# Kernel optimization log

Hardware: AMD Instinct MI355X
Metric: run time of the kernel (lower is better)

## Reference

```python
import jax, jax.numpy as jnp
import numpy as np

N_RAYS = 32768
N_SAMPLES = 1048576
HID = 64
STEP = 0.0005


def _mlp(x, W1, b1, W2, b2, W3, b3):
    h = jax.nn.relu(x @ W1 + b1)
    h = jax.nn.relu(h @ W2 + b2)
    return h @ W3 + b3


def setup_inputs() -> dict:
    key = jax.random.key(0)
    ks = jax.random.split(key, 12)
    rays_o = jax.random.normal(ks[0], (N_RAYS, 3), jnp.float32)
    rays_d = jax.random.normal(ks[1], (N_RAYS, 3), jnp.float32)
    rays_d = rays_d / jnp.linalg.norm(rays_d, axis=-1, keepdims=True)
    t_starts = jax.random.uniform(ks[2], (N_SAMPLES,), jnp.float32, 0.0, 1.5)
    t_ends = t_starts + STEP
    ray_indices = jnp.sort(jax.random.randint(ks[3], (N_SAMPLES,), 0, N_RAYS, jnp.int32))
    def lin(k, fin, fout):
        return jax.random.normal(k, (fin, fout), jnp.float32) / np.sqrt(fin)
    return {
        'rays_o': rays_o, 'rays_d': rays_d,
        't_starts': t_starts, 't_ends': t_ends,
        'ray_indices': ray_indices,
        'W_d1': lin(ks[4], 3, HID), 'b_d1': jnp.zeros((HID,), jnp.float32),
        'W_d2': lin(ks[5], HID, HID), 'b_d2': jnp.zeros((HID,), jnp.float32),
        'W_d3': lin(ks[6], HID, 1), 'b_d3': jnp.zeros((1,), jnp.float32),
        'W_r1': lin(ks[7], 3, HID), 'b_r1': jnp.zeros((HID,), jnp.float32),
        'W_r2': lin(ks[8], HID, HID), 'b_r2': jnp.zeros((HID,), jnp.float32),
        'W_r3': lin(ks[9], HID, 3), 'b_r3': jnp.zeros((3,), jnp.float32),
    }


def reference(rays_o, rays_d, t_starts, t_ends, ray_indices,
              W_d1, b_d1, W_d2, b_d2, W_d3, b_d3,
              W_r1, b_r1, W_r2, b_r2, W_r3, b_r3):
    n_rays = rays_o.shape[0]
    mid = (t_starts + t_ends) * 0.5                      # [S]
    # gather ray origins/dirs per sample, compute positions
    positions = rays_o[ray_indices] + rays_d[ray_indices] * mid[:, None]  # [S,3]
    # density query (NGP decoder stand-in), softplus activation like trunc_exp family
    sigmas = jax.nn.softplus(_mlp(positions, W_d1, b_d1, W_d2, b_d2, W_d3, b_d3))[:, 0]  # [S]
    # render_weight_from_density: segment-wise exclusive cumsum of sigma*dt
    sigma_dt = sigmas * (t_ends - t_starts)              # [S]
    excl_global = jnp.cumsum(sigma_dt) - sigma_dt        # global exclusive cumsum
    per_ray = jax.ops.segment_sum(sigma_dt, ray_indices, num_segments=n_rays)  # [R]
    ray_excl = jnp.cumsum(per_ray) - per_ray             # exclusive cumsum over rays
    within_excl = excl_global - ray_excl[ray_indices]    # exclusive within each ray
    trans = jnp.exp(-within_excl)                        # transmittance
    alphas = 1.0 - jnp.exp(-sigma_dt)
    weights = trans * alphas
    # accumulate_along_rays (scatter-sum over ray_indices)
    opacities = jax.ops.segment_sum(weights, ray_indices, num_segments=n_rays)[:, None]  # [R,1]
    distances = jax.ops.segment_sum(weights * mid, ray_indices, num_segments=n_rays)[:, None]
    # rgb query
    rgbs = jax.nn.sigmoid(_mlp(positions, W_r1, b_r1, W_r2, b_r2, W_r3, b_r3))  # [S,3]
    w_sg = jax.lax.stop_gradient(weights)
    colors = jax.ops.segment_sum(w_sg[:, None] * rgbs, ray_indices, num_segments=n_rays)  # [R,3]
    # eval-mode background composition (nerf.training == False branch)
    rest = jax.lax.stop_gradient(1.0 - opacities)
    distances = distances + 5.0 * rest
    colors = colors + 0.5 * rest
    return colors, distances, opacities
```

## Files before the change

kernel.cpp:

```cpp
#include <hip/hip_runtime.h>
#include <hip/hip_bf16.h>
#include <math.h>

#define N_RAYS   32768
#define N_SAMP   1048576
#define HID      64
#define ITERS    4
#define BLK_A    1024

typedef short bf8 __attribute__((ext_vector_type(8)));
typedef float f4  __attribute__((ext_vector_type(4)));

union BF8U { bf8 v; unsigned u[4]; };

static __device__ __forceinline__ unsigned bfbits(float x) {
    union { __bf16 h; unsigned short s; } c; c.h = (__bf16)x; return (unsigned)c.s;
}
static __device__ __forceinline__ unsigned pk2(float a, float b) {
#if __has_builtin(__builtin_amdgcn_cvt_pk_bf16_f32)
    return __builtin_bit_cast(unsigned, __builtin_amdgcn_cvt_pk_bf16_f32(a, b));
#else
    return bfbits(a) | (bfbits(b) << 16);
#endif
}
static __device__ __forceinline__ unsigned pk2r(float a, float b) {
    return pk2(fmaxf(a, 0.f), fmaxf(b, 0.f));
}
static __device__ __forceinline__ f4 mfma16(bf8 a, bf8 b, f4 c) {
    return __builtin_amdgcn_mfma_f32_16x16x32_bf16(a, b, c, 0, 0, 0);
}

__global__ __launch_bounds__(256, 2) void pass_a(
    const float* __restrict__ rays_o, const float* __restrict__ rays_d,
    const float* __restrict__ t_starts, const float* __restrict__ t_ends,
    const int*   __restrict__ ray_idx,
    const float* __restrict__ Wd1, const float* __restrict__ bd1,
    const float* __restrict__ Wd2, const float* __restrict__ bd2,
    const float* __restrict__ Wd3, const float* __restrict__ bd3,
    const float* __restrict__ Wr1, const float* __restrict__ br1,
    const float* __restrict__ Wr2, const float* __restrict__ br2,
    const float* __restrict__ Wr3, const float* __restrict__ br3,
    float4* __restrict__ ws4, int* __restrict__ start)
{
    const int lane = threadIdx.x & 63;
    const int wv   = (blockIdx.x * blockDim.x + threadIdx.x) >> 6;
    const int q    = lane >> 4;
    const int n    = lane & 15;
    const int qn   = n >> 2, rn = n & 3;
    const int rt   = n & 3;

    bf8 a1d[4], a1r[4];
    #pragma unroll
    for (int t = 0; t < 4; ++t) {
        const int row = 8*qn + 4*(t&1) + rn + 32*(t>>1);
        BF8U fd, fr;
        fd.u[0] = pk2(Wd1[row],       Wd1[HID+row]);
        fd.u[1] = pk2(Wd1[2*HID+row], bd1[row]);
        fd.u[2] = 0u; fd.u[3] = 0u;
        fr.u[0] = pk2(Wr1[row],       Wr1[HID+row]);
        fr.u[1] = pk2(Wr1[2*HID+row], br1[row]);
        fr.u[2] = 0u; fr.u[3] = 0u;
        a1d[t] = fd.v; a1r[t] = fr.v;
    }

    bf8 a2d[4][2], a2r[4][2];
    #pragma unroll
    for (int t = 0; t < 4; ++t) {
        const int row = 8*qn + 4*(t&1) + rn + 32*(t>>1);
        #pragma unroll
        for (int s = 0; s < 2; ++s) {
            BF8U fd, fr;
            #pragma unroll
            for (int dw = 0; dw < 4; ++dw) {
                const int k = 8*q + 2*dw + 32*s;
                fd.u[dw] = pk2(Wd2[k*HID+row], Wd2[(k+1)*HID+row]);
                fr.u[dw] = pk2(Wr2[k*HID+row], Wr2[(k+1)*HID+row]);
            }
            a2d[t][s] = fd.v; a2r[t][s] = fr.v;
        }
    }

    bf8 a3[4];
    #pragma unroll
    for (int s = 0; s < 4; ++s) {
        BF8U f;
        #pragma unroll
        for (int dw = 0; dw < 4; ++dw) {
            const int kg = 32*s + 8*q + 2*dw;
            float va = 0.f, vb = 0.f;
            if (rt == 0 && s < 2) { va = Wd3[kg]; vb = Wd3[kg+1]; }
            else if (rt >= 1 && s >= 2) {
                va = Wr3[(kg-64)*3 + (rt-1)];
                vb = Wr3[(kg-63)*3 + (rt-1)];
            }
            f.u[dw] = pk2(va, vb);
        }
        a3[s] = f.v;
    }

    f4 bias2d[4], bias2r[4];
    #pragma unroll
    for (int t = 0; t < 4; ++t) {
        #pragma unroll
        for (int rr = 0; rr < 4; ++rr) {
            const int row = 8*q + 4*(t&1) + rr + 32*(t>>1);
            bias2d[t][rr] = bd2[row];
            bias2r[t][rr] = br2[row];
        }
    }
    f4 bias3;
    #pragma unroll
    for (int rr = 0; rr < 4; ++rr)
        bias3[rr] = (rr == 0) ? bd3[0] : br3[rr-1];

    const int base0 = wv * (ITERS * 64);

    #pragma unroll 1
    for (int it = 0; it < ITERS; ++it) {
        const int base = base0 + it * 64;
        const int smp  = base + lane;

        const float ts = t_starts[smp], te = t_ends[smp];
        const int   ri = ray_idx[smp];
        const float mid = 0.5f*(ts+te), dt = te - ts;
        const float px = rays_o[3*ri+0] + rays_d[3*ri+0]*mid;
        const float py = rays_o[3*ri+1] + rays_d[3*ri+1]*mid;
        const float pz = rays_o[3*ri+2] + rays_d[3*ri+2]*mid;
        const unsigned p01 = pk2(px, py);
        const unsigned p23 = pk2(pz, 1.0f);

        int rp = __shfl_up(ri, 1, 64);
        if (lane == 0) rp = (smp == 0) ? -1 : ray_idx[smp-1];
        for (int rr = rp + 1; rr <= ri; ++rr) start[rr] = smp;
        if (smp == N_SAMP - 1)
            for (int rr = ri + 1; rr <= N_RAYS; ++rr) start[rr] = N_SAMP;

        f4 mine = {0.f, 0.f, 0.f, 0.f};

        #pragma unroll
        for (int u = 0; u < 4; ++u) {
            BF8U xb;
            xb.u[0] = (q == u) ? p01 : 0u;
            xb.u[1] = (q == u) ? p23 : 0u;
            xb.u[2] = 0u; xb.u[3] = 0u;

            const f4 zero = {0.f, 0.f, 0.f, 0.f};
            f4 d1d[4], d1r[4];
            #pragma unroll
            for (int t = 0; t < 4; ++t) {
                d1d[t] = mfma16(a1d[t], xb.v, zero);
                d1r[t] = mfma16(a1r[t], xb.v, zero);
            }

            bf8 b2d[2], b2r[2];
            #pragma unroll
            for (int s = 0; s < 2; ++s) {
                BF8U pd, pr;
                pd.u[0] = pk2r(d1d[2*s][0],   d1d[2*s][1]);
                pd.u[1] = pk2r(d1d[2*s][2],   d1d[2*s][3]);
                pd.u[2] = pk2r(d1d[2*s+1][0], d1d[2*s+1][1]);
                pd.u[3] = pk2r(d1d[2*s+1][2], d1d[2*s+1][3]);
                pr.u[0] = pk2r(d1r[2*s][0],   d1r[2*s][1]);
                pr.u[1] = pk2r(d1r[2*s][2],   d1r[2*s][3]);
                pr.u[2] = pk2r(d1r[2*s+1][0], d1r[2*s+1][1]);
                pr.u[3] = pk2r(d1r[2*s+1][2], d1r[2*s+1][3]);
                b2d[s] = pd.v; b2r[s] = pr.v;
            }

            f4 d2d[4], d2r[4];
            #pragma unroll
            for (int t = 0; t < 4; ++t) {
                f4 ad = bias2d[t];
                ad = mfma16(a2d[t][0], b2d[0], ad);
                ad = mfma16(a2d[t][1], b2d[1], ad);
                d2d[t] = ad;
                f4 ar = bias2r[t];
                ar = mfma16(a2r[t][0], b2r[0], ar);
                ar = mfma16(a2r[t][1], b2r[1], ar);
                d2r[t] = ar;
            }

            bf8 b3[4];
            #pragma unroll
            for (int s = 0; s < 2; ++s) {
                BF8U pd, pr;
                pd.u[0] = pk2r(d2d[2*s][0],   d2d[2*s][1]);
                pd.u[1] = pk2r(d2d[2*s][2],   d2d[2*s][3]);
                pd.u[2] = pk2r(d2d[2*s+1][0], d2d[2*s+1][1]);
                pd.u[3] = pk2r(d2d[2*s+1][2], d2d[2*s+1][3]);
                pr.u[0] = pk2r(d2r[2*s][0],   d2r[2*s][1]);
                pr.u[1] = pk2r(d2r[2*s][2],   d2r[2*s][3]);
                pr.u[2] = pk2r(d2r[2*s+1][0], d2r[2*s+1][1]);
                pr.u[3] = pk2r(d2r[2*s+1][2], d2r[2*s+1][3]);
                b3[s] = pd.v; b3[s+2] = pr.v;
            }

            f4 c3 = bias3;
            #pragma unroll
            for (int s = 0; s < 4; ++s) c3 = mfma16(a3[s], b3[s], c3);

            if (q == u) mine = c3;
        }

        const float sg = mine[0];
        const float sp = fmaxf(sg, 0.f) + __logf(1.f + __expf(-fabsf(sg)));
        const float sd = sp * dt;
        const float r0 = __builtin_amdgcn_rcpf(1.f + __expf(-mine[1]));
        const float g0 = __builtin_amdgcn_rcpf(1.f + __expf(-mine[2]));
        const float b0 = __builtin_amdgcn_rcpf(1.f + __expf(-mine[3]));
        ws4[smp] = make_float4(r0, g0, b0, sd);
    }
}

__global__ __launch_bounds__(256) void pass_b(
    const float* __restrict__ t_starts, const float* __restrict__ t_ends,
    const float4* __restrict__ ws4, const int* __restrict__ start,
    float* __restrict__ out)
{
    const int lane = threadIdx.x & 63;
    const int wv   = (blockIdx.x * blockDim.x + threadIdx.x) >> 6;
    const int half = lane >> 5;
    const int l32  = lane & 31;
    const int r    = 2*wv + half;
    if (r >= N_RAYS) return;

    int s0 = start[r], s1 = start[r+1];
    s0 = min(max(s0, 0), N_SAMP);
    s1 = min(max(s1, s0), N_SAMP);

    float cum = 0.f, opac = 0.f, dist = 0.f, c0 = 0.f, c1 = 0.f, c2 = 0.f;

    for (int base = s0; base < s1; base += 32) {
        int s = base + l32;
        bool ok = s < s1;
        float4 v  = ok ? ws4[s] : make_float4(0.f, 0.f, 0.f, 0.f);
        float mid = ok ? 0.5f*(t_starts[s] + t_ends[s]) : 0.f;
        float sd  = v.w;

        float x = sd;
        #pragma unroll
        for (int off = 1; off < 32; off <<= 1) {
            float y = __shfl_up(x, off, 32);
            if (l32 >= off) x += y;
        }
        float incl = cum + x;
        float excl = incl - sd;
        float w = __expf(-excl) - __expf(-incl);
        dist += w*mid; c0 += w*v.x; c1 += w*v.y; c2 += w*v.z;

        float tot = __shfl(x, 31, 32);
        opac += __expf(-cum) - __expf(-(cum + tot));
        cum  += tot;
    }

    #pragma unroll
    for (int off = 16; off > 0; off >>= 1) {
        dist += __shfl_xor(dist, off, 32);
        c0   += __shfl_xor(c0,   off, 32);
        c1   += __shfl_xor(c1,   off, 32);
        c2   += __shfl_xor(c2,   off, 32);
    }

    if (l32 == 0) {
        float rest = 1.f - opac;
        out[r*3 + 0] = c0 + 0.5f * rest;
        out[r*3 + 1] = c1 + 0.5f * rest;
        out[r*3 + 2] = c2 + 0.5f * rest;
        out[3*N_RAYS + r] = dist + 5.f * rest;
        out[4*N_RAYS + r] = opac;
    }
}

extern "C" void kernel_launch(void* const* d_in, const int* in_sizes, int n_in,
                              void* d_out, int out_size, void* d_ws, size_t ws_size,
                              hipStream_t stream) {
    const float* rays_o   = (const float*)d_in[0];
    const float* rays_d   = (const float*)d_in[1];
    const float* t_starts = (const float*)d_in[2];
    const float* t_ends   = (const float*)d_in[3];
    const int*   ray_idx  = (const int*)  d_in[4];
    const float* Wd1 = (const float*)d_in[5];  const float* bd1 = (const float*)d_in[6];
    const float* Wd2 = (const float*)d_in[7];  const float* bd2 = (const float*)d_in[8];
    const float* Wd3 = (const float*)d_in[9];  const float* bd3 = (const float*)d_in[10];
    const float* Wr1 = (const float*)d_in[11]; const float* br1 = (const float*)d_in[12];
    const float* Wr2 = (const float*)d_in[13]; const float* br2 = (const float*)d_in[14];
    const float* Wr3 = (const float*)d_in[15]; const float* br3 = (const float*)d_in[16];

    float4* ws4   = (float4*)d_ws;
    int*    start = (int*)((char*)d_ws + (size_t)N_SAMP * 16);
    float*  out   = (float*)d_out;

    hipLaunchKernelGGL(pass_a, dim3(BLK_A), dim3(256), 0, stream,
                       rays_o, rays_d, t_starts, t_ends, ray_idx,
                       Wd1, bd1, Wd2, bd2, Wd3, bd3,
                       Wr1, br1, Wr2, br2, Wr3, br3, ws4, start);

    hipLaunchKernelGGL(pass_b, dim3((N_RAYS/2 * 64) / 256), dim3(256), 0, stream,
                       t_starts, t_ends, ws4, start, out);
}
```

Before: 155.5 us.

## Split density and RGB MLPs into separate block halves with SoA workspace

Pass A now launches twice as many blocks: the first half evaluates only the density MLP, the second half only the RGB MLP, each for all samples. This halves per-thread weight registers and MFMA chains, which may improve occupancy and parallelism. The cost is recomputing sample positions twice and reading inputs twice. The workspace also changes from float4 AoS to four separate float arrays, so pass B now issues four scalar loads per sample.

```diff
diff --git a/kernel.cpp b/kernel.cpp
--- a/kernel.cpp
+++ b/kernel.cpp
@@ -6,7 +6,8 @@
 #define N_SAMP   1048576
 #define HID      64
 #define ITERS    4
-#define BLK_A    1024
+#define BLK_HALF 1024
+#define BLK_A    (2*BLK_HALF)
 
 typedef short bf8 __attribute__((ext_vector_type(8)));
 typedef float f4  __attribute__((ext_vector_type(4)));
@@ -40,78 +41,77 @@
     const float* __restrict__ Wr1, const float* __restrict__ br1,
     const float* __restrict__ Wr2, const float* __restrict__ br2,
     const float* __restrict__ Wr3, const float* __restrict__ br3,
-    float4* __restrict__ ws4, int* __restrict__ start)
+    float* __restrict__ ws_sd, float* __restrict__ ws_r,
+    float* __restrict__ ws_g,  float* __restrict__ ws_b,
+    int* __restrict__ start)
 {
-    const int lane = threadIdx.x & 63;
-    const int wv   = (blockIdx.x * blockDim.x + threadIdx.x) >> 6;
-    const int q    = lane >> 4;
-    const int n    = lane & 15;
-    const int qn   = n >> 2, rn = n & 3;
-    const int rt   = n & 3;
-
-    bf8 a1d[4], a1r[4];
+    const bool is_rgb = blockIdx.x >= BLK_HALF;
+    const int  blk    = is_rgb ? (blockIdx.x - BLK_HALF) : blockIdx.x;
+    const int  lane   = threadIdx.x & 63;
+    const int  wv     = ((blk << 8) + threadIdx.x) >> 6;
+    const int  q      = lane >> 4;
+    const int  n      = lane & 15;
+    const int  qn     = n >> 2, rn = n & 3;
+    const int  rt     = n & 3;
+
+    const float* W1 = is_rgb ? Wr1 : Wd1;  const float* b1 = is_rgb ? br1 : bd1;
+    const float* W2 = is_rgb ? Wr2 : Wd2;  const float* b2 = is_rgb ? br2 : bd2;
+    const float* W3 = is_rgb ? Wr3 : Wd3;  const float* b3 = is_rgb ? br3 : bd3;
+    const int    nc = is_rgb ? 3 : 1;
+    const int    ch = is_rgb ? (rt < 3 ? rt : 2) : 0;
+
+    bf8 a1[4];
     #pragma unroll
     for (int t = 0; t < 4; ++t) {
         const int row = 8*qn + 4*(t&1) + rn + 32*(t>>1);
-        BF8U fd, fr;
-        fd.u[0] = pk2(Wd1[row],       Wd1[HID+row]);
-        fd.u[1] = pk2(Wd1[2*HID+row], bd1[row]);
-        fd.u[2] = 0u; fd.u[3] = 0u;
-        fr.u[0] = pk2(Wr1[row],       Wr1[HID+row]);
-        fr.u[1] = pk2(Wr1[2*HID+row], br1[row]);
-        fr.u[2] = 0u; fr.u[3] = 0u;
-        a1d[t] = fd.v; a1r[t] = fr.v;
-    }
-
-    bf8 a2d[4][2], a2r[4][2];
+        BF8U f;
+        f.u[0] = pk2(W1[row],       W1[HID+row]);
+        f.u[1] = pk2(W1[2*HID+row], b1[row]);
+        f.u[2] = 0u; f.u[3] = 0u;
+        a1[t] = f.v;
+    }
+
+    bf8 a2[4][2];
     #pragma unroll
     for (int t = 0; t < 4; ++t) {
         const int row = 8*qn + 4*(t&1) + rn + 32*(t>>1);
         #pragma unroll
         for (int s = 0; s < 2; ++s) {
-            BF8U fd, fr;
+            BF8U f;
             #pragma unroll
             for (int dw = 0; dw < 4; ++dw) {
                 const int k = 8*q + 2*dw + 32*s;
-                fd.u[dw] = pk2(Wd2[k*HID+row], Wd2[(k+1)*HID+row]);
-                fr.u[dw] = pk2(Wr2[k*HID+row], Wr2[(k+1)*HID+row]);
-            }
-            a2d[t][s] = fd.v; a2r[t][s] = fr.v;
-        }
-    }
-
-    bf8 a3[4];
-    #pragma unroll
-    for (int s = 0; s < 4; ++s) {
+                f.u[dw] = pk2(W2[k*HID+row], W2[(k+1)*HID+row]);
+            }
+            a2[t][s] = f.v;
+        }
+    }
+
+    bf8 a3[2];
+    #pragma unroll
+    for (int s = 0; s < 2; ++s) {
         BF8U f;
         #pragma unroll
         for (int dw = 0; dw < 4; ++dw) {
             const int kg = 32*s + 8*q + 2*dw;
-            float va = 0.f, vb = 0.f;
-            if (rt == 0 && s < 2) { va = Wd3[kg]; vb = Wd3[kg+1]; }
-            else if (rt >= 1 && s >= 2) {
-                va = Wr3[(kg-64)*3 + (rt-1)];
-                vb = Wr3[(kg-63)*3 + (rt-1)];
-            }
-            f.u[dw] = pk2(va, vb);
+            f.u[dw] = pk2(W3[kg*nc + ch], W3[(kg+1)*nc + ch]);
         }
         a3[s] = f.v;
     }
 
-    f4 bias2d[4], bias2r[4];
+    f4 bias2[4];
     #pragma unroll
     for (int t = 0; t < 4; ++t) {
         #pragma unroll
         for (int rr = 0; rr < 4; ++rr) {
             const int row = 8*q + 4*(t&1) + rr + 32*(t>>1);
-            bias2d[t][rr] = bd2[row];
-            bias2r[t][rr] = br2[row];
+            bias2[t][rr] = b2[row];
         }
     }
     f4 bias3;
     #pragma unroll
     for (int rr = 0; rr < 4; ++rr)
-        bias3[rr] = (rr == 0) ? bd3[0] : br3[rr-1];
+        bias3[rr] = is_rgb ? b3[rr < 3 ? rr : 2] : b3[0];
 
     const int base0 = wv * (ITERS * 64);
 
@@ -129,11 +129,13 @@
         const unsigned p01 = pk2(px, py);
         const unsigned p23 = pk2(pz, 1.0f);
 
-        int rp = __shfl_up(ri, 1, 64);
-        if (lane == 0) rp = (smp == 0) ? -1 : ray_idx[smp-1];
-        for (int rr = rp + 1; rr <= ri; ++rr) start[rr] = smp;
-        if (smp == N_SAMP - 1)
-            for (int rr = ri + 1; rr <= N_RAYS; ++rr) start[rr] = N_SAMP;
+        if (!is_rgb) {
+            int rp = __shfl_up(ri, 1, 64);
+            if (lane == 0) rp = (smp == 0) ? -1 : ray_idx[smp-1];
+            for (int rr = rp + 1; rr <= ri; ++rr) start[rr] = smp;
+            if (smp == N_SAMP - 1)
+                for (int rr = ri + 1; rr <= N_RAYS; ++rr) start[rr] = N_SAMP;
+        }
 
         f4 mine = {0.f, 0.f, 0.f, 0.f};
 
@@ -145,77 +147,65 @@
             xb.u[2] = 0u; xb.u[3] = 0u;
 
             const f4 zero = {0.f, 0.f, 0.f, 0.f};
-            f4 d1d[4], d1r[4];
+            f4 d1[4];
+            #pragma unroll
+            for (int t = 0; t < 4; ++t) d1[t] = mfma16(a1[t], xb.v, zero);
+
+            bf8 bf2[2];
+            #pragma unroll
+            for (int s = 0; s < 2; ++s) {
+                BF8U p;
+                p.u[0] = pk2r(d1[2*s][0],   d1[2*s][1]);
+                p.u[1] = pk2r(d1[2*s][2],   d1[2*s][3]);
+                p.u[2] = pk2r(d1[2*s+1][0], d1[2*s+1][1]);
+                p.u[3] = pk2r(d1[2*s+1][2], d1[2*s+1][3]);
+                bf2[s] = p.v;
+            }
+
+            f4 d2[4];
             #pragma unroll
             for (int t = 0; t < 4; ++t) {
-                d1d[t] = mfma16(a1d[t], xb.v, zero);
-                d1r[t] = mfma16(a1r[t], xb.v, zero);
-            }
-
-            bf8 b2d[2], b2r[2];
+                f4 a = bias2[t];
+                a = mfma16(a2[t][0], bf2[0], a);
+                a = mfma16(a2[t][1], bf2[1], a);
+                d2[t] = a;
+            }
+
+            bf8 bf3[2];
             #pragma unroll
             for (int s = 0; s < 2; ++s) {
-                BF8U pd, pr;
-                pd.u[0] = pk2r(d1d[2*s][0],   d1d[2*s][1]);
-                pd.u[1] = pk2r(d1d[2*s][2],   d1d[2*s][3]);
-                pd.u[2] = pk2r(d1d[2*s+1][0], d1d[2*s+1][1]);
-                pd.u[3] = pk2r(d1d[2*s+1][2], d1d[2*s+1][3]);
-                pr.u[0] = pk2r(d1r[2*s][0],   d1r[2*s][1]);
-                pr.u[1] = pk2r(d1r[2*s][2],   d1r[2*s][3]);
-                pr.u[2] = pk2r(d1r[2*s+1][0], d1r[2*s+1][1]);
-                pr.u[3] = pk2r(d1r[2*s+1][2], d1r[2*s+1][3]);
-                b2d[s] = pd.v; b2r[s] = pr.v;
-            }
-
-            f4 d2d[4], d2r[4];
-            #pragma unroll
-            for (int t = 0; t < 4; ++t) {
-                f4 ad = bias2d[t];
-                ad = mfma16(a2d[t][0], b2d[0], ad);
-                ad = mfma16(a2d[t][1], b2d[1], ad);
-                d2d[t] = ad;
-                f4 ar = bias2r[t];
-                ar = mfma16(a2r[t][0], b2r[0], ar);
-                ar = mfma16(a2r[t][1], b2r[1], ar);
-                d2r[t] = ar;
-            }
-
-            bf8 b3[4];
-            #pragma unroll
-            for (int s = 0; s < 2; ++s) {
-                BF8U pd, pr;
-                pd.u[0] = pk2r(d2d[2*s][0],   d2d[2*s][1]);
-                pd.u[1] = pk2r(d2d[2*s][2],   d2d[2*s][3]);
-                pd.u[2] = pk2r(d2d[2*s+1][0], d2d[2*s+1][1]);
-                pd.u[3] = pk2r(d2d[2*s+1][2], d2d[2*s+1][3]);
-                pr.u[0] = pk2r(d2r[2*s][0],   d2r[2*s][1]);
-                pr.u[1] = pk2r(d2r[2*s][2],   d2r[2*s][3]);
-                pr.u[2] = pk2r(d2r[2*s+1][0], d2r[2*s+1][1]);
-                pr.u[3] = pk2r(d2r[2*s+1][2], d2r[2*s+1][3]);
-                b3[s] = pd.v; b3[s+2] = pr.v;
+                BF8U p;
+                p.u[0] = pk2r(d2[2*s][0],   d2[2*s][1]);
+                p.u[1] = pk2r(d2[2*s][2],   d2[2*s][3]);
+                p.u[2] = pk2r(d2[2*s+1][0], d2[2*s+1][1]);
+                p.u[3] = pk2r(d2[2*s+1][2], d2[2*s+1][3]);
+                bf3[s] = p.v;
             }
 
             f4 c3 = bias3;
-            #pragma unroll
-            for (int s = 0; s < 4; ++s) c3 = mfma16(a3[s], b3[s], c3);
+            c3 = mfma16(a3[0], bf3[0], c3);
+            c3 = mfma16(a3[1], bf3[1], c3);
 
             if (q == u) mine = c3;
         }
 
-        const float sg = mine[0];
-        const float sp = fmaxf(sg, 0.f) + __logf(1.f + __expf(-fabsf(sg)));
-        const float sd = sp * dt;
-        const float r0 = __builtin_amdgcn_rcpf(1.f + __expf(-mine[1]));
-        const float g0 = __builtin_amdgcn_rcpf(1.f + __expf(-mine[2]));
-        const float b0 = __builtin_amdgcn_rcpf(1.f + __expf(-mine[3]));
-        ws4[smp] = make_float4(r0, g0, b0, sd);
+        if (!is_rgb) {
+            const float sg = mine[0];
+            const float sp = fmaxf(sg, 0.f) + __logf(1.f + __expf(-fabsf(sg)));
+            ws_sd[smp] = sp * dt;
+        } else {
+            ws_r[smp] = __builtin_amdgcn_rcpf(1.f + __expf(-mine[0]));
+            ws_g[smp] = __builtin_amdgcn_rcpf(1.f + __expf(-mine[1]));
+            ws_b[smp] = __builtin_amdgcn_rcpf(1.f + __expf(-mine[2]));
+        }
     }
 }
 
 __global__ __launch_bounds__(256) void pass_b(
     const float* __restrict__ t_starts, const float* __restrict__ t_ends,
-    const float4* __restrict__ ws4, const int* __restrict__ start,
-    float* __restrict__ out)
+    const float* __restrict__ ws_sd, const float* __restrict__ ws_r,
+    const float* __restrict__ ws_g,  const float* __restrict__ ws_b,
+    const int* __restrict__ start, float* __restrict__ out)
 {
     const int lane = threadIdx.x & 63;
     const int wv   = (blockIdx.x * blockDim.x + threadIdx.x) >> 6;
@@ -233,9 +223,11 @@
     for (int base = s0; base < s1; base += 32) {
         int s = base + l32;
         bool ok = s < s1;
-        float4 v  = ok ? ws4[s] : make_float4(0.f, 0.f, 0.f, 0.f);
+        float sd  = ok ? ws_sd[s] : 0.f;
+        float vr  = ok ? ws_r[s]  : 0.f;
+        float vg  = ok ? ws_g[s]  : 0.f;
+        float vb  = ok ? ws_b[s]  : 0.f;
         float mid = ok ? 0.5f*(t_starts[s] + t_ends[s]) : 0.f;
-        float sd  = v.w;
 
         float x = sd;
         #pragma unroll
@@ -246,7 +238,7 @@
         float incl = cum + x;
         float excl = incl - sd;
         float w = __expf(-excl) - __expf(-incl);
-        dist += w*mid; c0 += w*v.x; c1 += w*v.y; c2 += w*v.z;
+        dist += w*mid; c0 += w*vr; c1 += w*vg; c2 += w*vb;
 
         float tot = __shfl(x, 31, 32);
         opac += __expf(-cum) - __expf(-(cum + tot));
@@ -286,15 +278,19 @@
     const float* Wr2 = (const float*)d_in[13]; const float* br2 = (const float*)d_in[14];
     const float* Wr3 = (const float*)d_in[15]; const float* br3 = (const float*)d_in[16];
 
-    float4* ws4   = (float4*)d_ws;
-    int*    start = (int*)((char*)d_ws + (size_t)N_SAMP * 16);
-    float*  out   = (float*)d_out;
+    float* ws_sd = (float*)d_ws;
+    float* ws_r  = ws_sd + N_SAMP;
+    float* ws_g  = ws_r  + N_SAMP;
+    float* ws_b  = ws_g  + N_SAMP;
+    int*   start = (int*)(ws_b + N_SAMP);
+    float* out   = (float*)d_out;
 
     hipLaunchKernelGGL(pass_a, dim3(BLK_A), dim3(256), 0, stream,
                        rays_o, rays_d, t_starts, t_ends, ray_idx,
                        Wd1, bd1, Wd2, bd2, Wd3, bd3,
-                       Wr1, br1, Wr2, br2, Wr3, br3, ws4, start);
+                       Wr1, br1, Wr2, br2, Wr3, br3,
+                       ws_sd, ws_r, ws_g, ws_b, start);
 
     hipLaunchKernelGGL(pass_b, dim3((N_RAYS/2 * 64) / 256), dim3(256), 0, stream,
-                       t_starts, t_ends, ws4, start, out);
-}
+                       t_starts, t_ends, ws_sd, ws_r, ws_g, ws_b, start, out);
+}
```

Result: faster. 147.9 us (-4.9%).
